# Kernel tuning notes

Measured on AMD Instinct MI355X. Metric: run time of the kernel, lower is better.

Reference implementation:

```python
import jax, jax.numpy as jnp
import numpy as np

N = 50000      # nodes
E = 800000     # edges (avg degree 16)
IN = 128; HID = 128; OUT = 128; HEADS = 4
NEG_SLOPE = 0.2


def setup_inputs() -> dict:
    key = jax.random.key(0)
    ks = jax.random.split(key, 16)
    def glorot(k, shape):
        fan = shape[0] if len(shape) == 2 else int(np.prod(shape))
        return jax.random.normal(k, shape, jnp.float32) * np.float32(1.0 / np.sqrt(fan))
    C = HID // HEADS
    x = jax.random.normal(ks[0], (N, IN), jnp.float32)
    edge_index = jax.random.randint(ks[1], (2, E), 0, N, jnp.int32)
    return {
        "x": x, "edge_index": edge_index,
        "W1": glorot(ks[2], (IN, HID)),  "as1": glorot(ks[3], (HEADS, C)),  "ad1": glorot(ks[4], (HEADS, C)),  "b1": jnp.zeros((HID,), jnp.float32),
        "W2": glorot(ks[5], (HID, HID)), "as2": glorot(ks[6], (HEADS, C)),  "ad2": glorot(ks[7], (HEADS, C)),  "b2": jnp.zeros((HID,), jnp.float32),
        "W3": glorot(ks[8], (HID, OUT)), "as3": glorot(ks[9], (1, OUT)),    "ad3": glorot(ks[10], (1, OUT)),   "b3": jnp.zeros((OUT,), jnp.float32),
    }


def gat_conv(x, ei, W, a_src, a_dst, b, concat):
    # x: [N,Fin], ei: [2,E'] (self-loops included), W: [Fin, H*C], a_*: [H,C]
    n = x.shape[0]
    H, C = a_src.shape
    h = (x @ W).reshape(n, H, C)                         # [N,H,C]
    src, dst = ei[0], ei[1]
    alpha_s = jnp.einsum('nhc,hc->nh', h, a_src)         # [N,H]
    alpha_d = jnp.einsum('nhc,hc->nh', h, a_dst)
    e = jax.nn.leaky_relu(alpha_s[src] + alpha_d[dst], NEG_SLOPE)  # [E',H]
    # segment softmax over destination neighborhoods
    m = jax.ops.segment_max(e, dst, num_segments=n)      # [N,H]
    p = jnp.exp(e - m[dst])
    denom = jax.ops.segment_sum(p, dst, num_segments=n)  # [N,H]
    alpha = p / (denom[dst] + 1e-16)                     # [E',H]
    out = jax.ops.segment_sum(h[src] * alpha[:, :, None], dst, num_segments=n)  # [N,H,C]
    out = out.reshape(n, H * C) if concat else out.mean(axis=1)
    return out + b


def reference(x, edge_index, W1, as1, ad1, b1, W2, as2, ad2, b2, W3, as3, ad3, b3):
    n = x.shape[0]
    loops = jnp.arange(n, dtype=edge_index.dtype)
    ei = jnp.concatenate([edge_index, jnp.stack([loops, loops])], axis=1)  # add self-loops
    h = jax.nn.relu(gat_conv(x, ei, W1, as1, ad1, b1, True))   # dropout p=0 / eval: identity
    h = jax.nn.relu(gat_conv(h, ei, W2, as2, ad2, b2, True))
    return gat_conv(h, ei, W3, as3, ad3, b3, False)
```

## Files before the change

kernel.cpp:

```cpp
#include <hip/hip_runtime.h>
#include <hip/hip_bf16.h>
#include <math.h>

#define SB 1024

typedef __attribute__((ext_vector_type(8))) short bf16x8;
typedef __attribute__((ext_vector_type(4))) float f32x4;

__device__ __forceinline__ float lrelu(float v) { return fmaxf(v, 0.2f * v); }

__device__ __forceinline__ unsigned fenc(float f) {
    unsigned u = __float_as_uint(f);
    return (u & 0x80000000u) ? ~u : (u | 0x80000000u);
}
__device__ __forceinline__ float fdec(unsigned u) {
    return __uint_as_float((u & 0x80000000u) ? (u & 0x7FFFFFFFu) : ~u);
}
__device__ __forceinline__ unsigned short f2bf(float f) {
    union { __hip_bfloat16 b; unsigned short u; } cv;
    cv.b = __float2bfloat16(f);
    return cv.u;
}
__device__ __forceinline__ float bflo(unsigned u) { return __uint_as_float(u << 16); }
__device__ __forceinline__ float bfhi(unsigned u) { return __uint_as_float(u & 0xFFFF0000u); }


__global__ void setup_all(const float* __restrict__ x,
                          const float* __restrict__ W1, const float* __restrict__ W2,
                          const float* __restrict__ W3,
                          unsigned short* __restrict__ xb,
                          unsigned short* __restrict__ Wt1, unsigned short* __restrict__ Wt2,
                          unsigned short* __restrict__ Wt3,
                          int* __restrict__ cursor, unsigned short* __restrict__ srcs,
                          unsigned* __restrict__ gmax, unsigned short* __restrict__ hb,
                          int N, int GX) {
    int b = blockIdx.x, t = threadIdx.x;
    if (b < GX) {
        int i = b * 256 + t;
        if (i < N * 32) {
            float4 v = ((const float4*)x)[i];
            ushort4 o;
            o.x = f2bf(v.x); o.y = f2bf(v.y); o.z = f2bf(v.z); o.w = f2bf(v.w);
            ((ushort4*)xb)[i] = o;
        }
        if (i < N) {
            cursor[i] = (i << 6) + 1;
            srcs[(size_t)i << 6] = (unsigned short)i;
        }
        if (i < 12) gmax[i] = fenc(-1e30f);
        if (i < 64) ((unsigned*)hb)[(size_t)N * 64 + i] = 0;
        return;
    }
    {
        int j = (b - GX) * 256 + t;
        if (j < 3 * 16384) {
            int mm = j >> 14, e = j & 16383;
            const float* W = (mm == 0) ? W1 : (mm == 1) ? W2 : W3;
            unsigned short* Wt = (mm == 0) ? Wt1 : (mm == 1) ? Wt2 : Wt3;
            int k = e >> 7, c = e & 127;
            Wt[c * 128 + k] = f2bf(W[e]);
        }
    }
}


__device__ __forceinline__ void scatter_body(int sb, int t, const int* __restrict__ ei,
                                             int E, int N, int* cursor,
                                             unsigned short* __restrict__ srcs, int pn) {
    int part = sb & 7;
    int chunk = sb >> 3;
    int stride = (SB >> 3) * 256;
    int lo = part * pn, hi = min(lo + pn, N);
    for (int i = chunk * 256 + t; i < E; i += stride) {
        int d = ei[E + i];
        if (d >= lo && d < hi) {
            int pos = atomicAdd(&cursor[d], 1);
            if (pos - (d << 6) < 64) srcs[pos] = (unsigned short)ei[i];
        }
    }
}

__device__ __forceinline__ void pad_body(int pb, int t, int* __restrict__ cursor,
                                         unsigned short* __restrict__ srcs, int N) {
    int n = pb * 256 + t;
    if (n >= N) return;
    int dr = cursor[n] - (n << 6);
    if (dr > 64) dr = 64;
    int q = (dr + 3) >> 2;
    for (int k = dr; k < q * 4; k++) srcs[(n << 6) + k] = (unsigned short)N;
    cursor[n] = q;
}


template <int H>
__device__ __forceinline__ void gemm_body(int bid, const unsigned short* __restrict__ xb,
                                          const unsigned short* __restrict__ Wt,
                                          const float* __restrict__ a_s,
                                          const float* __restrict__ a_d,
                                          unsigned short* __restrict__ hb,
                                          float* __restrict__ asb,
                                          float* __restrict__ adb,
                                          unsigned* __restrict__ gmax, int N) {
    constexpr int HH = (H == 4) ? 4 : 1;
    __shared__ float smax[4][HH];
    int t = threadIdx.x;
    int wave = t >> 6, lane = t & 63;
    int lrow = lane & 15;
    int kg = lane >> 4;
    int row0 = bid * 64 + wave * 16;
    int arow = min(row0 + lrow, N - 1);
    const bf16x8* ap = (const bf16x8*)(xb + (size_t)arow * 128 + kg * 8);

    f32x4 acc[8];
#pragma unroll
    for (int ct = 0; ct < 8; ct++) acc[ct] = (f32x4)0.f;
#pragma unroll
    for (int kk = 0; kk < 4; kk++) {
        bf16x8 a = ap[kk * 4];
#pragma unroll
        for (int ct = 0; ct < 8; ct++) {
            const bf16x8* bp = (const bf16x8*)(Wt + (size_t)(ct * 16 + lrow) * 128 + kk * 32 + kg * 8);
            acc[ct] = __builtin_amdgcn_mfma_f32_16x16x32_bf16(a, *bp, acc[ct], 0, 0, 0);
        }
    }
    int orow = row0 + kg * 4;
#pragma unroll
    for (int reg = 0; reg < 4; reg++) {
        int r = orow + reg;
        if (r < N) {
#pragma unroll
            for (int ct = 0; ct < 8; ct++)
                hb[(size_t)r * 128 + ct * 16 + lrow] = f2bf(acc[ct][reg]);
        }
    }
    float ps[4][HH], pd[4][HH];
#pragma unroll
    for (int reg = 0; reg < 4; reg++)
#pragma unroll
        for (int hd = 0; hd < HH; hd++) { ps[reg][hd] = 0.f; pd[reg][hd] = 0.f; }
#pragma unroll
    for (int ct = 0; ct < 8; ct++) {
        int hd = (H == 4) ? (ct >> 1) : 0;
        float asv = a_s[ct * 16 + lrow];
        float adv = a_d[ct * 16 + lrow];
#pragma unroll
        for (int reg = 0; reg < 4; reg++) {
            ps[reg][hd] += acc[ct][reg] * asv;
            pd[reg][hd] += acc[ct][reg] * adv;
        }
    }
    for (int o = 1; o < 16; o <<= 1) {
#pragma unroll
        for (int reg = 0; reg < 4; reg++)
#pragma unroll
            for (int hd = 0; hd < HH; hd++) {
                ps[reg][hd] += __shfl_xor(ps[reg][hd], o);
                pd[reg][hd] += __shfl_xor(pd[reg][hd], o);
            }
    }
    if (lrow < HH) {
        int hd = lrow;
#pragma unroll
        for (int reg = 0; reg < 4; reg++) {
            int r = orow + reg;
            if (r < N) {
                asb[(size_t)r * H + hd] = ps[reg][hd];
                adb[(size_t)r * H + hd] = pd[reg][hd];
            }
        }
    }
    float wm[HH];
#pragma unroll
    for (int hd = 0; hd < HH; hd++) {
        float m = fmaxf(fmaxf(ps[0][hd], ps[1][hd]), fmaxf(ps[2][hd], ps[3][hd]));
        m = fmaxf(m, __shfl_xor(m, 16));
        m = fmaxf(m, __shfl_xor(m, 32));
        wm[hd] = m;
    }
    if (lane == 0)
#pragma unroll
        for (int hd = 0; hd < HH; hd++) smax[wave][hd] = wm[hd];
    __syncthreads();
    if (t < HH) {
        float m = fmaxf(fmaxf(smax[0][t], smax[1][t]), fmaxf(smax[2][t], smax[3][t]));
        atomicMax(&gmax[t], fenc(m));
    }
    if (bid == 0 && t == 0) {
#pragma unroll
        for (int hd = 0; hd < HH; hd++) asb[(size_t)N * H + hd] = -1e30f;
    }
}


__global__ __launch_bounds__(256) void gemm1_scatter(const unsigned short* __restrict__ xb,
                                                     const unsigned short* __restrict__ Wt,
                                                     const float* __restrict__ a_s,
                                                     const float* __restrict__ a_d,
                                                     unsigned short* __restrict__ hb,
                                                     float* __restrict__ asb,
                                                     float* __restrict__ adb,
                                                     unsigned* __restrict__ gmax,
                                                     const int* __restrict__ ei, int E,
                                                     int* __restrict__ cursor,
                                                     unsigned short* __restrict__ srcs,
                                                     int N, int gb, int pn) {
    if ((int)blockIdx.x < gb)
        gemm_body<4>(blockIdx.x, xb, Wt, a_s, a_d, hb, asb, adb, gmax, N);
    else
        scatter_body(blockIdx.x - gb, threadIdx.x, ei, E, N, cursor, srcs, pn);
}

__global__ __launch_bounds__(256) void gemm2_pad(const unsigned short* __restrict__ xb,
                                                 const unsigned short* __restrict__ Wt,
                                                 const float* __restrict__ a_s,
                                                 const float* __restrict__ a_d,
                                                 unsigned short* __restrict__ hb,
                                                 float* __restrict__ asb,
                                                 float* __restrict__ adb,
                                                 unsigned* __restrict__ gmax,
                                                 int* __restrict__ cursor,
                                                 unsigned short* __restrict__ srcs,
                                                 int N, int gb) {
    if ((int)blockIdx.x < gb)
        gemm_body<4>(blockIdx.x, xb, Wt, a_s, a_d, hb, asb, adb, gmax, N);
    else
        pad_body(blockIdx.x - gb, threadIdx.x, cursor, srcs, N);
}

__global__ __launch_bounds__(256) void gemm3_k(const unsigned short* __restrict__ xb,
                                               const unsigned short* __restrict__ Wt,
                                               const float* __restrict__ a_s,
                                               const float* __restrict__ a_d,
                                               unsigned short* __restrict__ hb,
                                               float* __restrict__ asb,
                                               float* __restrict__ adb,
                                               unsigned* __restrict__ gmax, int N) {
    gemm_body<1>(blockIdx.x, xb, Wt, a_s, a_d, hb, asb, adb, gmax, N);
}


template <int H, bool RELU, bool OUTBF, bool MASK>
__global__ __launch_bounds__(256) void aggregate10(const unsigned short* __restrict__ hb,
                                                   const unsigned short* __restrict__ srcs,
                                                   const int* __restrict__ qn,
                                                   const float* __restrict__ asb,
                                                   const float* __restrict__ adb,
                                                   const unsigned* __restrict__ gmax,
                                                   const float* __restrict__ bias,
                                                   void* __restrict__ outv, int N) {
    int n = (blockIdx.x * 256 + threadIdx.x) >> 4;
    if (n >= N) return;
    unsigned l = threadIdx.x & 15;
    unsigned ht = (H == 4) ? (l >> 2) : 0;
    int base = (threadIdx.x & 63) & ~15;
    float adn = adb[(unsigned)n * H + ht];
    float m = lrelu(fdec(gmax[ht]) + adn);
    const unsigned short* sp = srcs + ((size_t)n << 6);
    const uint4* hrow = (const uint4*)hb;
    int cv = qn[n];
    int nb, rem;
    if (MASK) {
        int dr = cv - (n << 6);
        dr = min(dr, 64);
        nb = (dr + 3) >> 2;
        rem = dr - ((nb - 1) << 2);
    } else {
        nb = cv;
        rem = 4;
    }
    float a0 = 0.f, a1 = 0.f, a2 = 0.f, a3 = 0.f;
    float a4 = 0.f, a5 = 0.f, a6 = 0.f, a7 = 0.f, den = 0.f;

    ushort4 sq = *(const ushort4*)sp;
    uint4 u0 = hrow[(unsigned)sq.x * 16u + l];
    uint4 u1 = hrow[(unsigned)sq.y * 16u + l];
    uint4 u2 = hrow[(unsigned)sq.z * 16u + l];
    uint4 u3 = hrow[(unsigned)sq.w * 16u + l];
    for (int j = 0; j < nb; j++) {
        int jn = (j + 1 < nb) ? j + 1 : j;
        ushort4 sn = *(const ushort4*)(sp + jn * 4);
        uint4 v0 = hrow[(unsigned)sn.x * 16u + l];
        uint4 v1 = hrow[(unsigned)sn.y * 16u + l];
        uint4 v2 = hrow[(unsigned)sn.z * 16u + l];
        uint4 v3 = hrow[(unsigned)sn.w * 16u + l];
        unsigned sown = sp[j * 4 + (l & 3)];
        float e = asb[sown * H + ht];
        float pown = __expf(lrelu(e + adn) - m);
        float p0 = __shfl(pown, base + (int)ht * 4 + 0);
        float p1 = __shfl(pown, base + (int)ht * 4 + 1);
        float p2 = __shfl(pown, base + (int)ht * 4 + 2);
        float p3 = __shfl(pown, base + (int)ht * 4 + 3);
        if (MASK) {
            int limit = (j == nb - 1) ? rem : 4;
            p1 = (1 < limit) ? p1 : 0.f;
            p2 = (2 < limit) ? p2 : 0.f;
            p3 = (3 < limit) ? p3 : 0.f;
        }
        a0 += p0 * bflo(u0.x); a1 += p0 * bfhi(u0.x); a2 += p0 * bflo(u0.y); a3 += p0 * bfhi(u0.y);
        a4 += p0 * bflo(u0.z); a5 += p0 * bfhi(u0.z); a6 += p0 * bflo(u0.w); a7 += p0 * bfhi(u0.w);
        a0 += p1 * bflo(u1.x); a1 += p1 * bfhi(u1.x); a2 += p1 * bflo(u1.y); a3 += p1 * bfhi(u1.y);
        a4 += p1 * bflo(u1.z); a5 += p1 * bfhi(u1.z); a6 += p1 * bflo(u1.w); a7 += p1 * bfhi(u1.w);
        a0 += p2 * bflo(u2.x); a1 += p2 * bfhi(u2.x); a2 += p2 * bflo(u2.y); a3 += p2 * bfhi(u2.y);
        a4 += p2 * bflo(u2.z); a5 += p2 * bfhi(u2.z); a6 += p2 * bflo(u2.w); a7 += p2 * bfhi(u2.w);
        a0 += p3 * bflo(u3.x); a1 += p3 * bfhi(u3.x); a2 += p3 * bflo(u3.y); a3 += p3 * bfhi(u3.y);
        a4 += p3 * bflo(u3.z); a5 += p3 * bfhi(u3.z); a6 += p3 * bflo(u3.w); a7 += p3 * bfhi(u3.w);
        den += p0 + p1 + p2 + p3;
        sq = sn; u0 = v0; u1 = v1; u2 = v2; u3 = v3;
    }
    float inv = 1.f / (den + 1e-16f);
    unsigned c = l * 8;
    float4 bv0 = *(const float4*)&bias[c];
    float4 bv1 = *(const float4*)&bias[c + 4];
    float o0 = a0 * inv + bv0.x, o1 = a1 * inv + bv0.y;
    float o2 = a2 * inv + bv0.z, o3 = a3 * inv + bv0.w;
    float o4 = a4 * inv + bv1.x, o5 = a5 * inv + bv1.y;
    float o6 = a6 * inv + bv1.z, o7 = a7 * inv + bv1.w;
    if (RELU) {
        o0 = fmaxf(o0, 0.f); o1 = fmaxf(o1, 0.f); o2 = fmaxf(o2, 0.f); o3 = fmaxf(o3, 0.f);
        o4 = fmaxf(o4, 0.f); o5 = fmaxf(o5, 0.f); o6 = fmaxf(o6, 0.f); o7 = fmaxf(o7, 0.f);
    }
    if (OUTBF) {
        uint4 st;
        st.x = (unsigned)f2bf(o0) | ((unsigned)f2bf(o1) << 16);
        st.y = (unsigned)f2bf(o2) | ((unsigned)f2bf(o3) << 16);
        st.z = (unsigned)f2bf(o4) | ((unsigned)f2bf(o5) << 16);
        st.w = (unsigned)f2bf(o6) | ((unsigned)f2bf(o7) << 16);
        *(uint4*)&((unsigned short*)outv)[(size_t)n * 128 + c] = st;
    } else {
        float* op = (float*)outv + (size_t)n * 128 + c;
        float4 s0; s0.x = o0; s0.y = o1; s0.z = o2; s0.w = o3;
        float4 s1; s1.x = o4; s1.y = o5; s1.z = o6; s1.w = o7;
        *(float4*)op = s0;
        *(float4*)(op + 4) = s1;
    }
}


extern "C" void kernel_launch(void* const* d_in, const int* in_sizes, int n_in,
                              void* d_out, int out_size, void* d_ws, size_t ws_size,
                              hipStream_t stream) {
    const float* x   = (const float*)d_in[0];
    const int*   ei  = (const int*)d_in[1];
    const float* W1  = (const float*)d_in[2];
    const float* as1 = (const float*)d_in[3];
    const float* ad1 = (const float*)d_in[4];
    const float* b1  = (const float*)d_in[5];
    const float* W2  = (const float*)d_in[6];
    const float* as2 = (const float*)d_in[7];
    const float* ad2 = (const float*)d_in[8];
    const float* b2  = (const float*)d_in[9];
    const float* W3  = (const float*)d_in[10];
    const float* as3 = (const float*)d_in[11];
    const float* ad3 = (const float*)d_in[12];
    const float* b3  = (const float*)d_in[13];

    const int N = in_sizes[0] / 128;
    const int E = in_sizes[1] / 2;
    const int PN = (N + 7) / 8;

    char* w = (char*)d_ws;
    size_t woff = 0;
    auto alloc = [&](size_t bytes) -> void* {
        void* p = w + woff;
        woff = (woff + bytes + 255) & ~(size_t)255;
        return p;
    };
    int*      cursor = (int*)alloc((size_t)(N + 1) * 4);
    unsigned short* srcs = (unsigned short*)alloc(((size_t)N * 64 + 64) * 2);
    float*    asb    = (float*)alloc((size_t)(N + 1) * 4 * 4);
    float*    adb    = (float*)alloc((size_t)(N + 1) * 4 * 4);
    unsigned* gmax   = (unsigned*)alloc(16 * 4);
    unsigned short* hb  = (unsigned short*)alloc((size_t)(N + 1) * 128 * 2);
    unsigned short* xb  = (unsigned short*)alloc((size_t)N * 128 * 2);
    unsigned short* Wt1 = (unsigned short*)alloc(128 * 128 * 2);
    unsigned short* Wt2 = (unsigned short*)alloc(128 * 128 * 2);
    unsigned short* Wt3 = (unsigned short*)alloc(128 * 128 * 2);
    float* outf = (float*)d_out;

    const int GX = (N * 32 + 255) / 256;
    const int gb = (N + 63) / 64;
    const int ga = (N * 16 + 255) / 256;
    const int PB = (N + 255) / 256;

    setup_all<<<GX + 192, 256, 0, stream>>>(x, W1, W2, W3, xb, Wt1, Wt2, Wt3,
                                            cursor, srcs, gmax, hb, N, GX);

    gemm1_scatter<<<gb + SB, 256, 0, stream>>>(xb, Wt1, as1, ad1, hb, asb, adb, gmax + 0,
                                               ei, E, cursor, srcs, N, gb, PN);

    aggregate10<4, true, true, true><<<ga, 256, 0, stream>>>(hb, srcs, cursor, asb, adb,
                                                             gmax + 0, b1, xb, N);

    gemm2_pad<<<gb + PB, 256, 0, stream>>>(xb, Wt2, as2, ad2, hb, asb, adb, gmax + 4,
                                           cursor, srcs, N, gb);

    aggregate10<4, true, true, false><<<ga, 256, 0, stream>>>(hb, srcs, cursor, asb, adb,
                                                              gmax + 4, b2, xb, N);

    gemm3_k<<<gb, 256, 0, stream>>>(xb, Wt3, as3, ad3, hb, asb, adb, gmax + 8, N);

    aggregate10<1, false, false, false><<<ga, 256, 0, stream>>>(hb, srcs, cursor, asb, adb,
                                                                gmax + 8, b3, outf, N);
}
```

Measured before the change: 235.9 us.

## Make GEMM persistent with register-resident weights and LDS-staged vectorized epilogue

The per-block GEMM becomes a persistent grid of 512 blocks. Each wave loads the full 128x128 bf16 weight matrix into registers once, then loops over 16-row tiles and prefetches the next A tile. Results are staged through LDS so each lane owns a contiguous row slice. That lane computes the attention dot products and writes the bf16 row with 16-byte stores instead of scattered 2-byte stores. The 128 weight vector registers and launch_bounds(256,2) raise register pressure and may cause spills or reduce occupancy.

```diff
diff --git a/kernel.cpp b/kernel.cpp
--- a/kernel.cpp
+++ b/kernel.cpp
@@ -3,6 +3,7 @@
 #include <math.h>
 
 #define SB 1024
+#define GB 512
 
 typedef __attribute__((ext_vector_type(8))) short bf16x8;
 typedef __attribute__((ext_vector_type(4))) float f32x4;
@@ -80,6 +81,7 @@
     }
 }
 
+
 __device__ __forceinline__ void pad_body(int pb, int t, int* __restrict__ cursor,
                                          unsigned short* __restrict__ srcs, int N) {
     int n = pb * 256 + t;
@@ -93,149 +95,194 @@
 
 
 template <int H>
-__device__ __forceinline__ void gemm_body(int bid, const unsigned short* __restrict__ xb,
-                                          const unsigned short* __restrict__ Wt,
-                                          const float* __restrict__ a_s,
-                                          const float* __restrict__ a_d,
-                                          unsigned short* __restrict__ hb,
-                                          float* __restrict__ asb,
-                                          float* __restrict__ adb,
-                                          unsigned* __restrict__ gmax, int N) {
+__device__ __forceinline__ void gemm_body2(int wid, int nwaves, int wave,
+                                           const unsigned short* __restrict__ xb,
+                                           const unsigned short* __restrict__ Wt,
+                                           const float* __restrict__ a_s,
+                                           const float* __restrict__ a_d,
+                                           unsigned short* __restrict__ hb,
+                                           float* __restrict__ asb,
+                                           float* __restrict__ adb,
+                                           unsigned* __restrict__ gmax,
+                                           float* __restrict__ wlds,
+                                           float (*smax)[4], int N) {
     constexpr int HH = (H == 4) ? 4 : 1;
-    __shared__ float smax[4][HH];
-    int t = threadIdx.x;
-    int wave = t >> 6, lane = t & 63;
+    int lane = threadIdx.x & 63;
     int lrow = lane & 15;
     int kg = lane >> 4;
-    int row0 = bid * 64 + wave * 16;
-    int arow = min(row0 + lrow, N - 1);
-    const bf16x8* ap = (const bf16x8*)(xb + (size_t)arow * 128 + kg * 8);
-
-    f32x4 acc[8];
-#pragma unroll
-    for (int ct = 0; ct < 8; ct++) acc[ct] = (f32x4)0.f;
-#pragma unroll
-    for (int kk = 0; kk < 4; kk++) {
-        bf16x8 a = ap[kk * 4];
-#pragma unroll
-        for (int ct = 0; ct < 8; ct++) {
-            const bf16x8* bp = (const bf16x8*)(Wt + (size_t)(ct * 16 + lrow) * 128 + kk * 32 + kg * 8);
-            acc[ct] = __builtin_amdgcn_mfma_f32_16x16x32_bf16(a, *bp, acc[ct], 0, 0, 0);
-        }
-    }
-    int orow = row0 + kg * 4;
-#pragma unroll
-    for (int reg = 0; reg < 4; reg++) {
-        int r = orow + reg;
-        if (r < N) {
+
+    bf16x8 B[32];
+#pragma unroll
+    for (int ct = 0; ct < 8; ct++)
+#pragma unroll
+        for (int kk = 0; kk < 4; kk++)
+            B[ct * 4 + kk] = *(const bf16x8*)(Wt + (size_t)(ct * 16 + lrow) * 128 + kk * 32 + kg * 8);
+
+    int ntiles = (N + 15) >> 4;
+    float wmax = -1e30f;
+
+    bf16x8 A[4];
+    {
+        int tt = (wid < ntiles) ? wid : 0;
+        int arow = min(tt * 16 + lrow, N - 1);
+        const bf16x8* ap = (const bf16x8*)(xb + (size_t)arow * 128 + kg * 8);
+        A[0] = ap[0]; A[1] = ap[4]; A[2] = ap[8]; A[3] = ap[12];
+    }
+
+    for (int t = wid; t < ntiles; t += nwaves) {
+        bf16x8 An[4];
+        {
+            int tn = (t + nwaves < ntiles) ? t + nwaves : t;
+            int arow = min(tn * 16 + lrow, N - 1);
+            const bf16x8* ap = (const bf16x8*)(xb + (size_t)arow * 128 + kg * 8);
+            An[0] = ap[0]; An[1] = ap[4]; An[2] = ap[8]; An[3] = ap[12];
+        }
+        f32x4 acc[8];
+#pragma unroll
+        for (int ct = 0; ct < 8; ct++) acc[ct] = (f32x4)0.f;
+#pragma unroll
+        for (int kk = 0; kk < 4; kk++)
 #pragma unroll
             for (int ct = 0; ct < 8; ct++)
-                hb[(size_t)r * 128 + ct * 16 + lrow] = f2bf(acc[ct][reg]);
-        }
-    }
-    float ps[4][HH], pd[4][HH];
-#pragma unroll
-    for (int reg = 0; reg < 4; reg++)
-#pragma unroll
-        for (int hd = 0; hd < HH; hd++) { ps[reg][hd] = 0.f; pd[reg][hd] = 0.f; }
-#pragma unroll
-    for (int ct = 0; ct < 8; ct++) {
-        int hd = (H == 4) ? (ct >> 1) : 0;
-        float asv = a_s[ct * 16 + lrow];
-        float adv = a_d[ct * 16 + lrow];
-#pragma unroll
-        for (int reg = 0; reg < 4; reg++) {
-            ps[reg][hd] += acc[ct][reg] * asv;
-            pd[reg][hd] += acc[ct][reg] * adv;
-        }
-    }
-    for (int o = 1; o < 16; o <<= 1) {
-#pragma unroll
-        for (int reg = 0; reg < 4; reg++)
-#pragma unroll
-            for (int hd = 0; hd < HH; hd++) {
-                ps[reg][hd] += __shfl_xor(ps[reg][hd], o);
-                pd[reg][hd] += __shfl_xor(pd[reg][hd], o);
+                acc[ct] = __builtin_amdgcn_mfma_f32_16x16x32_bf16(A[kk], B[ct * 4 + kk], acc[ct], 0, 0, 0);
+
+#pragma unroll
+        for (int ct = 0; ct < 8; ct++)
+#pragma unroll
+            for (int reg = 0; reg < 4; reg++)
+                wlds[(kg * 4 + reg) * 132 + ct * 16 + lrow] = acc[ct][reg];
+
+        const float* rp = wlds + lrow * 132 + kg * 32;
+        const float* asp = a_s + kg * 32;
+        const float* adp = a_d + kg * 32;
+        float hv[32];
+        float s = 0.f, d = 0.f;
+#pragma unroll
+        for (int q = 0; q < 8; q++) {
+            float4 v = *(const float4*)(rp + q * 4);
+            float4 av = *(const float4*)(asp + q * 4);
+            float4 dv = *(const float4*)(adp + q * 4);
+            hv[q * 4 + 0] = v.x; hv[q * 4 + 1] = v.y; hv[q * 4 + 2] = v.z; hv[q * 4 + 3] = v.w;
+            s += v.x * av.x + v.y * av.y + v.z * av.z + v.w * av.w;
+            d += v.x * dv.x + v.y * dv.y + v.z * dv.z + v.w * dv.w;
+        }
+        if (H == 1) {
+            s += __shfl_xor(s, 16); s += __shfl_xor(s, 32);
+            d += __shfl_xor(d, 16); d += __shfl_xor(d, 32);
+        }
+        int r = t * 16 + lrow;
+        bool valid = r < N;
+        if (valid) {
+            if (H == 4) {
+                asb[(size_t)r * 4 + kg] = s;
+                adb[(size_t)r * 4 + kg] = d;
+            } else if (kg == 0) {
+                asb[r] = s;
+                adb[r] = d;
             }
-    }
-    if (lrow < HH) {
-        int hd = lrow;
-#pragma unroll
-        for (int reg = 0; reg < 4; reg++) {
-            int r = orow + reg;
-            if (r < N) {
-                asb[(size_t)r * H + hd] = ps[reg][hd];
-                adb[(size_t)r * H + hd] = pd[reg][hd];
-            }
-        }
-    }
-    float wm[HH];
-#pragma unroll
-    for (int hd = 0; hd < HH; hd++) {
-        float m = fmaxf(fmaxf(ps[0][hd], ps[1][hd]), fmaxf(ps[2][hd], ps[3][hd]));
-        m = fmaxf(m, __shfl_xor(m, 16));
-        m = fmaxf(m, __shfl_xor(m, 32));
-        wm[hd] = m;
-    }
-    if (lane == 0)
-#pragma unroll
-        for (int hd = 0; hd < HH; hd++) smax[wave][hd] = wm[hd];
+        }
+        wmax = fmaxf(wmax, valid ? s : -1e30f);
+        unsigned st[16];
+#pragma unroll
+        for (int q = 0; q < 16; q++)
+            st[q] = (unsigned)f2bf(hv[2 * q]) | ((unsigned)f2bf(hv[2 * q + 1]) << 16);
+        if (valid) {
+            uint4* dst = (uint4*)(hb + (size_t)r * 128 + kg * 32);
+            uint4 s0; s0.x = st[0];  s0.y = st[1];  s0.z = st[2];  s0.w = st[3];
+            uint4 s1; s1.x = st[4];  s1.y = st[5];  s1.z = st[6];  s1.w = st[7];
+            uint4 s2; s2.x = st[8];  s2.y = st[9];  s2.z = st[10]; s2.w = st[11];
+            uint4 s3; s3.x = st[12]; s3.y = st[13]; s3.z = st[14]; s3.w = st[15];
+            dst[0] = s0; dst[1] = s1; dst[2] = s2; dst[3] = s3;
+        }
+#pragma unroll
+        for (int q = 0; q < 4; q++) A[q] = An[q];
+    }
+
+    if (H == 4) {
+        wmax = fmaxf(wmax, __shfl_xor(wmax, 1));
+        wmax = fmaxf(wmax, __shfl_xor(wmax, 2));
+        wmax = fmaxf(wmax, __shfl_xor(wmax, 4));
+        wmax = fmaxf(wmax, __shfl_xor(wmax, 8));
+        if (lrow == 0) smax[wave][kg] = wmax;
+    } else {
+        wmax = fmaxf(wmax, __shfl_xor(wmax, 1));
+        wmax = fmaxf(wmax, __shfl_xor(wmax, 2));
+        wmax = fmaxf(wmax, __shfl_xor(wmax, 4));
+        wmax = fmaxf(wmax, __shfl_xor(wmax, 8));
+        wmax = fmaxf(wmax, __shfl_xor(wmax, 16));
+        wmax = fmaxf(wmax, __shfl_xor(wmax, 32));
+        if (lane == 0) smax[wave][0] = wmax;
+    }
     __syncthreads();
-    if (t < HH) {
-        float m = fmaxf(fmaxf(smax[0][t], smax[1][t]), fmaxf(smax[2][t], smax[3][t]));
-        atomicMax(&gmax[t], fenc(m));
-    }
-    if (bid == 0 && t == 0) {
+    if (threadIdx.x < HH) {
+        float m = fmaxf(fmaxf(smax[0][threadIdx.x], smax[1][threadIdx.x]),
+                        fmaxf(smax[2][threadIdx.x], smax[3][threadIdx.x]));
+        atomicMax(&gmax[threadIdx.x], fenc(m));
+    }
+    if (wid == 0 && threadIdx.x == 0) {
 #pragma unroll
         for (int hd = 0; hd < HH; hd++) asb[(size_t)N * H + hd] = -1e30f;
     }
 }
 
 
-__global__ __launch_bounds__(256) void gemm1_scatter(const unsigned short* __restrict__ xb,
-                                                     const unsigned short* __restrict__ Wt,
-                                                     const float* __restrict__ a_s,
-                                                     const float* __restrict__ a_d,
-                                                     unsigned short* __restrict__ hb,
-                                                     float* __restrict__ asb,
-                                                     float* __restrict__ adb,
-                                                     unsigned* __restrict__ gmax,
-                                                     const int* __restrict__ ei, int E,
-                                                     int* __restrict__ cursor,
-                                                     unsigned short* __restrict__ srcs,
-                                                     int N, int gb, int pn) {
-    if ((int)blockIdx.x < gb)
-        gemm_body<4>(blockIdx.x, xb, Wt, a_s, a_d, hb, asb, adb, gmax, N);
-    else
-        scatter_body(blockIdx.x - gb, threadIdx.x, ei, E, N, cursor, srcs, pn);
-}
-
-__global__ __launch_bounds__(256) void gemm2_pad(const unsigned short* __restrict__ xb,
-                                                 const unsigned short* __restrict__ Wt,
-                                                 const float* __restrict__ a_s,
-                                                 const float* __restrict__ a_d,
-                                                 unsigned short* __restrict__ hb,
-                                                 float* __restrict__ asb,
-                                                 float* __restrict__ adb,
-                                                 unsigned* __restrict__ gmax,
-                                                 int* __restrict__ cursor,
-                                                 unsigned short* __restrict__ srcs,
-                                                 int N, int gb) {
-    if ((int)blockIdx.x < gb)
-        gemm_body<4>(blockIdx.x, xb, Wt, a_s, a_d, hb, asb, adb, gmax, N);
-    else
-        pad_body(blockIdx.x - gb, threadIdx.x, cursor, srcs, N);
-}
-
-__global__ __launch_bounds__(256) void gemm3_k(const unsigned short* __restrict__ xb,
-                                               const unsigned short* __restrict__ Wt,
-                                               const float* __restrict__ a_s,
-                                               const float* __restrict__ a_d,
-                                               unsigned short* __restrict__ hb,
-                                               float* __restrict__ asb,
-                                               float* __restrict__ adb,
-                                               unsigned* __restrict__ gmax, int N) {
-    gemm_body<1>(blockIdx.x, xb, Wt, a_s, a_d, hb, asb, adb, gmax, N);
+__global__ __launch_bounds__(256, 2) void gemm1_scatter(const unsigned short* __restrict__ xb,
+                                                        const unsigned short* __restrict__ Wt,
+                                                        const float* __restrict__ a_s,
+                                                        const float* __restrict__ a_d,
+                                                        unsigned short* __restrict__ hb,
+                                                        float* __restrict__ asb,
+                                                        float* __restrict__ adb,
+                                                        unsigned* __restrict__ gmax,
+                                                        const int* __restrict__ ei, int E,
+                                                        int* __restrict__ cursor,
+                                                        unsigned short* __restrict__ srcs,
+                                                        int N, int pn) {
+    __shared__ float lds[4][16 * 132];
+    __shared__ float smax[4][4];
+    if ((int)blockIdx.x < GB) {
+        int wave = threadIdx.x >> 6;
+        gemm_body2<4>(blockIdx.x * 4 + wave, GB * 4, wave, xb, Wt, a_s, a_d,
+                      hb, asb, adb, gmax, lds[wave], smax, N);
+    } else {
+        scatter_body(blockIdx.x - GB, threadIdx.x, ei, E, N, cursor, srcs, pn);
+    }
+}
+
+__global__ __launch_bounds__(256, 2) void gemm2_pad(const unsigned short* __restrict__ xb,
+                                                    const unsigned short* __restrict__ Wt,
+                                                    const float* __restrict__ a_s,
+                                                    const float* __restrict__ a_d,
+                                                    unsigned short* __restrict__ hb,
+                                                    float* __restrict__ asb,
+                                                    float* __restrict__ adb,
+                                                    unsigned* __restrict__ gmax,
+                                                    int* __restrict__ cursor,
+                                                    unsigned short* __restrict__ srcs, int N) {
+    __shared__ float lds[4][16 * 132];
+    __shared__ float smax[4][4];
+    if ((int)blockIdx.x < GB) {
+        int wave = threadIdx.x >> 6;
+        gemm_body2<4>(blockIdx.x * 4 + wave, GB * 4, wave, xb, Wt, a_s, a_d,
+                      hb, asb, adb, gmax, lds[wave], smax, N);
+    } else {
+        pad_body(blockIdx.x - GB, threadIdx.x, cursor, srcs, N);
+    }
+}
+
+__global__ __launch_bounds__(256, 2) void gemm3_k(const unsigned short* __restrict__ xb,
+                                                  const unsigned short* __restrict__ Wt,
+                                                  const float* __restrict__ a_s,
+                                                  const float* __restrict__ a_d,
+                                                  unsigned short* __restrict__ hb,
+                                                  float* __restrict__ asb,
+                                                  float* __restrict__ adb,
+                                                  unsigned* __restrict__ gmax, int N) {
+    __shared__ float lds[4][16 * 132];
+    __shared__ float smax[4][4];
+    int wave = threadIdx.x >> 6;
+    gemm_body2<1>(blockIdx.x * 4 + wave, GB * 4, wave, xb, Wt, a_s, a_d,
+                  hb, asb, adb, gmax, lds[wave], smax, N);
 }
 
 
@@ -378,26 +425,25 @@
     float* outf = (float*)d_out;
 
     const int GX = (N * 32 + 255) / 256;
-    const int gb = (N + 63) / 64;
     const int ga = (N * 16 + 255) / 256;
     const int PB = (N + 255) / 256;
 
     setup_all<<<GX + 192, 256, 0, stream>>>(x, W1, W2, W3, xb, Wt1, Wt2, Wt3,
                                             cursor, srcs, gmax, hb, N, GX);
 
-    gemm1_scatter<<<gb + SB, 256, 0, stream>>>(xb, Wt1, as1, ad1, hb, asb, adb, gmax + 0,
-                                               ei, E, cursor, srcs, N, gb, PN);
+    gemm1_scatter<<<GB + SB, 256, 0, stream>>>(xb, Wt1, as1, ad1, hb, asb, adb, gmax + 0,
+                                               ei, E, cursor, srcs, N, PN);
 
     aggregate10<4, true, true, true><<<ga, 256, 0, stream>>>(hb, srcs, cursor, asb, adb,
                                                              gmax + 0, b1, xb, N);
 
-    gemm2_pad<<<gb + PB, 256, 0, stream>>>(xb, Wt2, as2, ad2, hb, asb, adb, gmax + 4,
-                                           cursor, srcs, N, gb);
+    gemm2_pad<<<GB + PB, 256, 0, stream>>>(xb, Wt2, as2, ad2, hb, asb, adb, gmax + 4,
+                                           cursor, srcs, N);
 
     aggregate10<4, true, true, false><<<ga, 256, 0, stream>>>(hb, srcs, cursor, asb, adb,
                                                               gmax + 4, b2, xb, N);
 
-    gemm3_k<<<gb, 256, 0, stream>>>(xb, Wt3, as3, ad3, hb, asb, adb, gmax + 8, N);
+    gemm3_k<<<GB, 256, 0, stream>>>(xb, Wt3, as3, ad3, hb, asb, adb, gmax + 8, N);
 
     aggregate10<1, false, false, false><<<ga, 256, 0, stream>>>(hb, srcs, cursor, asb, adb,
                                                                 gmax + 8, b3, outf, N);
```

Measured after the change: 231.0 us. -2.1%, faster.
